# Kernel optimization log

Measured on AMD Instinct MI355X. Metric: run time of the kernel, lower is better.

The kernel has to match this reference:

```python
import jax, jax.numpy as jnp
import numpy as np

EMBED_DIM = 1024
NUM_HEADS = 16
HEAD_DIM = EMBED_DIM // NUM_HEADS
WINDOW = 128  # window_size: attend to [i-W, i+W]


def setup_inputs() -> dict:
    key = jax.random.key(0)
    ks = jax.random.split(key, 9)
    B, S, E = 4, 4096, EMBED_DIM
    s = 1.0 / np.sqrt(E)
    return {
        "x": jax.random.normal(ks[0], (B, S, E), jnp.float32),
        "Wq": jax.random.normal(ks[1], (E, E), jnp.float32) * s,
        "bq": jnp.zeros((E,), jnp.float32),
        "Wk": jax.random.normal(ks[2], (E, E), jnp.float32) * s,
        "bk": jnp.zeros((E,), jnp.float32),
        "Wv": jax.random.normal(ks[3], (E, E), jnp.float32) * s,
        "bv": jnp.zeros((E,), jnp.float32),
        "Wo": jax.random.normal(ks[4], (E, E), jnp.float32) * s,
        "bo": jnp.zeros((E,), jnp.float32),
    }


def reference(x, Wq, bq, Wk, bk, Wv, bv, Wo, bo):
    B, S, E = x.shape
    H, D, W = NUM_HEADS, HEAD_DIM, WINDOW
    scale = jnp.sqrt(jnp.asarray(D, x.dtype))

    def heads(t):  # [B,S,E] -> [B,H,S,D]
        return t.reshape(B, S, H, D).transpose(0, 2, 1, 3)

    q = heads(x @ Wq + bq)
    k = heads(x @ Wk + bk)
    v = heads(x @ Wv + bv)

    # window indices per query position: j = i + [-W..W], masked to [0, S)
    offs = jnp.arange(-W, W + 1)                 # [2W+1]
    idx = jnp.arange(S)[:, None] + offs[None, :]  # [S, 2W+1]
    valid = (idx >= 0) & (idx < S)
    idxc = jnp.clip(idx, 0, S - 1)

    k_win = k[:, :, idxc, :]  # [B,H,S,2W+1,D]
    v_win = v[:, :, idxc, :]

    scores = jnp.einsum('bhsd,bhswd->bhsw', q, k_win) / scale
    scores = jnp.where(valid[None, None], scores, jnp.asarray(-jnp.inf, scores.dtype))
    attn = jax.nn.softmax(scores, axis=-1)
    out = jnp.einsum('bhsw,bhswd->bhsd', attn, v_win)  # [B,H,S,D]

    out = out.transpose(0, 2, 1, 3).reshape(B, S, E)
    return out @ Wo + bo
```

## Files before the change

kernel.cpp:

```cpp
#include <hip/hip_runtime.h>
#include <hip/hip_bf16.h>
#include <type_traits>

typedef unsigned short u16;
typedef __attribute__((ext_vector_type(8))) short  s16x8;
typedef __attribute__((ext_vector_type(4))) short  s16x4;
typedef __attribute__((ext_vector_type(8))) __bf16 b16x8;
typedef __attribute__((ext_vector_type(4))) float  f32x4;

#define S_LEN 4096
#define NB    4
#define EMB   1024
#define NH    16
#define HD    64
#define NROWS (NB * S_LEN)
#define KDIM  1024
#define BHSTRIDE (S_LEN * HD)

static __device__ __forceinline__ u16 f2b(float f) {
  __hip_bfloat16 h = __float2bfloat16(f);
  return __builtin_bit_cast(u16, h);
}

template <typename T, typename = void>
struct mfma_takes : std::false_type {};
template <typename T>
struct mfma_takes<T, std::void_t<decltype(__builtin_amdgcn_mfma_f32_16x16x32_bf16(
    std::declval<T>(), std::declval<T>(), std::declval<f32x4>(), 0, 0, 0))>> : std::true_type {};

template <typename AB>
static __device__ __forceinline__ f32x4 mfma_any(AB a, AB b, f32x4 c) {
  return __builtin_amdgcn_mfma_f32_16x16x32_bf16(a, b, c, 0, 0, 0);
}

template <typename S8 = s16x8, typename B8 = b16x8>
static __device__ __forceinline__ f32x4 MFMA_BF16(s16x8 a, s16x8 b, f32x4 c) {
  if constexpr (mfma_takes<S8>::value)
    return mfma_any<S8>(__builtin_bit_cast(S8, a), __builtin_bit_cast(S8, b), c);
  else
    return mfma_any<B8>(__builtin_bit_cast(B8, a), __builtin_bit_cast(B8, b), c);
}

static __device__ __forceinline__ void gld_lds16(const void* g, void* l) {
  __builtin_amdgcn_global_load_lds((const __attribute__((address_space(1))) void*)g,
                                   (__attribute__((address_space(3))) void*)l, 16, 0, 0);
}

__global__ __launch_bounds__(256) void cvt_x_kernel(const float* __restrict__ in,
                                                    u16* __restrict__ out) {
  long i = ((long)blockIdx.x * 256 + threadIdx.x) * 8;
  float4 a = *(const float4*)(in + i);
  float4 b = *(const float4*)(in + i + 4);
  s16x8 o;
  o[0] = (short)f2b(a.x); o[1] = (short)f2b(a.y); o[2] = (short)f2b(a.z); o[3] = (short)f2b(a.w);
  o[4] = (short)f2b(b.x); o[5] = (short)f2b(b.y); o[6] = (short)f2b(b.z); o[7] = (short)f2b(b.w);
  *(s16x8*)(out + i) = o;
}

__global__ __launch_bounds__(256) void transpose_cvt4_kernel(
    const float* __restrict__ W0, const float* __restrict__ W1,
    const float* __restrict__ W2, const float* __restrict__ W3,
    u16* __restrict__ D0, u16* __restrict__ D1, u16* __restrict__ D2, u16* __restrict__ D3) {
  __shared__ float tile[32][33];
  const float* W; u16* D;
  switch (blockIdx.z) {
    case 0:  W = W0; D = D0; break;
    case 1:  W = W1; D = D1; break;
    case 2:  W = W2; D = D2; break;
    default: W = W3; D = D3; break;
  }
  int n0 = blockIdx.x * 32, k0 = blockIdx.y * 32;
  int tx = threadIdx.x & 31, ty = threadIdx.x >> 5;
#pragma unroll
  for (int i = ty; i < 32; i += 8)
    tile[i][tx] = W[(long)(k0 + i) * EMB + n0 + tx];
  __syncthreads();
#pragma unroll
  for (int i = ty; i < 32; i += 8)
    D[(long)(n0 + i) * EMB + k0 + tx] = f2b(tile[tx][i]);
}

#define SA_(p,k) (((p)*2+(k))*8192)
#define SB_(p,k) (32768 + ((p)*2+(k))*8192)

__global__ __launch_bounds__(512, 2) void gemm8p_kernel(
    const u16* __restrict__ A, const u16* __restrict__ Bt,
    const float* __restrict__ b0, const float* __restrict__ b1, const float* __restrict__ b2,
    void* __restrict__ Cp, u16* __restrict__ Qb, u16* __restrict__ Kp, u16* __restrict__ Vt,
    int N, int out_f32) {
  __shared__ __align__(16) u16 smem[65536];
  const int tid = threadIdx.x;
  const int w = tid >> 6, lane = tid & 63;
  const int wm = w >> 2, wn = w & 3;
  const int frow = lane & 15, fg = lane >> 4;

  const int nwg = gridDim.x;
  const int bid = ((int)blockIdx.x & 7) * (nwg >> 3) + ((int)blockIdx.x >> 3);
  const int nbn = N >> 8;
  const int bm = bid / nbn, bn = bid % nbn;

  int offA[8];
#pragma unroll
  for (int j = 0; j < 8; j++) {
    int row = wm * 128 + j * 16 + frow;
    offA[j] = row * 32 + ((fg ^ ((row ^ (row >> 2)) & 3)) << 3);
  }
  int offB[4];
#pragma unroll
  for (int j = 0; j < 4; j++) {
    int row = wn * 64 + j * 16 + frow;
    offB[j] = row * 32 + ((fg ^ ((row ^ (row >> 2)) & 3)) << 3);
  }
  int srow[2], soff[2];
#pragma unroll
  for (int L = 0; L < 2; L++) {
    int lin = L * 512 + tid;
    int r = lin >> 2;
    srow[L] = r;
    soff[L] = (((lin & 3) ^ ((r ^ (r >> 2)) & 3)) << 3);
  }
  const u16* Abase = A + (long)bm * 256 * KDIM;
  const u16* Bbase = Bt + (long)bn * 256 * KDIM;

  f32x4 acc[8][4];
#pragma unroll
  for (int m = 0; m < 8; m++)
#pragma unroll
    for (int n = 0; n < 4; n++) acc[m][n] = (f32x4)0.0f;

  auto STAGE = [&](const u16* gb, int kcol, int slot) {
#pragma unroll
    for (int L = 0; L < 2; L++)
      gld_lds16(gb + (long)srow[L] * KDIM + kcol + soff[L],
                &smem[slot + (L * 512 + w * 64) * 8]);
  };

  s16x8 af[4], bf[4];

  STAGE(Abase, 0,  SA_(0,0)); STAGE(Bbase, 0,  SB_(0,0));
  STAGE(Abase, 32, SA_(0,1)); STAGE(Bbase, 32, SB_(0,1));
  STAGE(Abase, 64, SA_(1,0)); STAGE(Bbase, 64, SB_(1,0));
  asm volatile("s_waitcnt vmcnt(8)" ::: "memory");
  asm volatile("s_barrier" ::: "memory");

#define PHASE(p, k, mh, RDB, GB, KCOL, SLOT, DOVM)                            \
  {                                                                           \
    if (RDB) {                                                                \
      _Pragma("unroll") for (int n = 0; n < 4; n++)                           \
        bf[n] = *(const s16x8*)&smem[SB_(p, k) + offB[n]];                    \
    }                                                                         \
    _Pragma("unroll") for (int m = 0; m < 4; m++)                             \
      af[m] = *(const s16x8*)&smem[SA_(p, k) + offA[(mh) * 4 + m]];           \
    STAGE(GB, KCOL, SLOT);                                                    \
    asm volatile("s_barrier" ::: "memory");                                   \
    asm volatile("s_waitcnt lgkmcnt(0)" ::: "memory");                        \
    __builtin_amdgcn_sched_barrier(0);                                        \
    __builtin_amdgcn_s_setprio(1);                                            \
    _Pragma("unroll") for (int m = 0; m < 4; m++)                             \
      _Pragma("unroll") for (int n = 0; n < 4; n++)                           \
        acc[(mh) * 4 + m][n] = MFMA_BF16(af[m], bf[n], acc[(mh) * 4 + m][n]); \
    __builtin_amdgcn_s_setprio(0);                                            \
    if (DOVM) asm volatile("s_waitcnt vmcnt(8)" ::: "memory");                \
    asm volatile("s_barrier" ::: "memory");                                   \
  }

#pragma unroll 1
  for (int i = 0; i < 8; i++) {
    const int t = 2 * i;
    const int k1 = ((t + 1) & 15) * 64;
    const int k2 = ((t + 2) & 15) * 64;
    const int k3 = ((t + 3) & 15) * 64;
    PHASE(0, 0, 0, 1, Abase, k1 + 32, SA_(1, 1), 0)
    PHASE(0, 0, 1, 0, Bbase, k1 + 32, SB_(1, 1), 1)
    PHASE(0, 1, 0, 1, Abase, k2,      SA_(0, 0), 0)
    PHASE(0, 1, 1, 0, Bbase, k2,      SB_(0, 0), 1)
    PHASE(1, 0, 0, 1, Abase, k2 + 32, SA_(0, 1), 0)
    PHASE(1, 0, 1, 0, Bbase, k2 + 32, SB_(0, 1), 1)
    PHASE(1, 1, 0, 1, Abase, k3,      SA_(1, 0), 0)
    PHASE(1, 1, 1, 0, Bbase, k3,      SB_(1, 0), 1)
  }
#undef PHASE

  asm volatile("s_waitcnt vmcnt(0) lgkmcnt(0)" ::: "memory");
  asm volatile("s_barrier" ::: "memory");

  const int Mbase = bm * 256 + wm * 128;

  if (!out_f32) {
    const int g = bn * 256 + wn * 64;
    const int part = g >> 10;
    const int head = (g & 1023) >> 6;
    const float* bias = (part == 0) ? b0 : ((part == 1) ? b1 : b2);
    float bv[4];
#pragma unroll
    for (int n = 0; n < 4; n++) bv[n] = bias[(g & 1023) + n * 16 + frow];
    u16* buf = &smem[w * 2048];
#pragma unroll
    for (int mf2 = 0; mf2 < 4; mf2++) {
#pragma unroll
      for (int half = 0; half < 2; half++) {
        const int mf = mf2 * 2 + half;
#pragma unroll
        for (int n = 0; n < 4; n++)
#pragma unroll
          for (int r = 0; r < 4; r++) {
            int row32 = half * 16 + 4 * fg + r;
            int col = n * 16 + frow;
            buf[row32 * 64 + (((col >> 3) ^ (row32 & 7)) << 3) + (col & 7)] =
                f2b(acc[mf][n][r] + bv[n]);
          }
      }
      asm volatile("s_waitcnt lgkmcnt(0)" ::: "memory");
      __builtin_amdgcn_sched_barrier(0);
      const int s0 = Mbase + mf2 * 32;
      if (part == 2) {
        const int d = lane;
        u16 tmp[32];
#pragma unroll
        for (int r32 = 0; r32 < 32; r32++)
          tmp[r32] = buf[r32 * 64 + (((d >> 3) ^ (r32 & 7)) << 3) + (d & 7)];
        u16* dst = Vt + ((long)((s0 >> 12) * 16 + head)) * BHSTRIDE + (long)d * S_LEN + (s0 & 4095);
#pragma unroll
        for (int q = 0; q < 4; q++) {
          s16x8 pk;
#pragma unroll
          for (int j = 0; j < 8; j++) pk[j] = (short)tmp[q * 8 + j];
          *(s16x8*)(dst + q * 8) = pk;
        }
      } else {
#pragma unroll
        for (int i = 0; i < 4; i++) {
          int flat = lane + 64 * i;
          int row32 = flat >> 3, ch = flat & 7;
          s16x8 v = *(const s16x8*)&buf[row32 * 64 + ((ch ^ (row32 & 7)) << 3)];
          int s = s0 + row32;
          u16* dst = (part == 0)
              ? (Qb + (long)s * 1024 + head * 64 + ch * 8)
              : (Kp + ((long)(s >> 12) * 16 + head) * BHSTRIDE + (long)(s & 4095) * 64 + ch * 8);
          *(s16x8*)dst = v;
        }
      }
      asm volatile("s_waitcnt lgkmcnt(0)" ::: "memory");
      __builtin_amdgcn_sched_barrier(0);
    }
  } else {
    float* fbuf = (float*)&smem[w * 2048];
    const long crow0 = (long)Mbase * N + bn * 256 + wn * 64;
#pragma unroll
    for (int mf = 0; mf < 8; mf++) {
#pragma unroll
      for (int n = 0; n < 4; n++) {
        float bvv = b0[(bn * 256 + wn * 64 + n * 16 + frow) & 1023];
#pragma unroll
        for (int r = 0; r < 4; r++) {
          int row = 4 * fg + r;
          int o = 4 * n + (frow >> 2);
          fbuf[row * 64 + ((o ^ (row & 7)) << 2) + (frow & 3)] = acc[mf][n][r] + bvv;
        }
      }
      asm volatile("s_waitcnt lgkmcnt(0)" ::: "memory");
      __builtin_amdgcn_sched_barrier(0);
#pragma unroll
      for (int i = 0; i < 4; i++) {
        int flat = lane + 64 * i;
        int row = flat >> 4, oct = lane & 15;
        float4 v = *(const float4*)&fbuf[row * 64 + ((oct ^ (row & 7)) << 2)];
        *(float4*)((float*)Cp + crow0 + (long)(mf * 16 + row) * N + oct * 4) = v;
      }
      asm volatile("s_waitcnt lgkmcnt(0)" ::: "memory");
      __builtin_amdgcn_sched_barrier(0);
    }
  }
}

#define QBLK 128

__global__ __launch_bounds__(256) void attn_kernel(const u16* __restrict__ Qb,
                                                   const u16* __restrict__ Kp,
                                                   const u16* __restrict__ Vt,
                                                   u16* __restrict__ Oa) {
  __shared__ __align__(16) u16 smem[16384];

  const int tid = threadIdx.x;
  const int w = tid >> 6, lane = tid & 63;
  const int frow = lane & 15, fg = lane >> 4;

  const int nq = S_LEN / QBLK;
  int bid = (int)blockIdx.x;
  bid = (bid & 7) * ((NB * NH * nq) >> 3) + (bid >> 3);
  const int b = bid / (NH * nq);
  const int rem = bid % (NH * nq);
  const int h = rem / nq;
  const int qt = rem % nq;
  const int q0 = qt * QBLK;
  const int qw0 = q0 + 32 * w;

  const u16* Kpb = Kp + (long)(b * NH + h) * BHSTRIDE;
  const u16* Vtb = Vt + (long)(b * NH + h) * BHSTRIDE;

  s16x8 qf[2][2];
#pragma unroll
  for (int m = 0; m < 2; m++)
#pragma unroll
    for (int kk = 0; kk < 2; kk++)
      qf[m][kk] = *(const s16x8*)(Qb + (long)(b * S_LEN + qw0 + 16 * m + frow) * 1024 +
                                  h * 64 + kk * 32 + 8 * fg);

  f32x4 acc[2][4];
#pragma unroll
  for (int m = 0; m < 2; m++)
#pragma unroll
    for (int n = 0; n < 4; n++) acc[m][n] = (f32x4)0.0f;
  float mrow[2] = {-1e30f, -1e30f};
  float lrow[2] = {0.f, 0.f};

  const int r8 = lane >> 3;
  const int cs = ((lane & 7) ^ r8) << 3;

  auto STAGE = [&](int kvb, int bufi) {
#pragma unroll
    for (int pass = 0; pass < 2; pass++) {
      int rbase = pass * 32 + w * 8;
      gld_lds16(Kpb + (long)(kvb + rbase + r8) * 64 + cs, &smem[bufi * 4096 + rbase * 64]);
      gld_lds16(Vtb + (long)(rbase + r8) * S_LEN + kvb + cs, &smem[8192 + bufi * 4096 + rbase * 64]);
    }
  };

  const int tlo = (q0 == 0) ? 2 : 0;
  const int thi = (q0 == S_LEN - QBLK) ? 3 : 5;

  STAGE(q0 - 128 + 64 * tlo, 0);

#pragma unroll 1
  for (int t = tlo; t <= thi; t++) {
    const int cur = (t - tlo) & 1;
    const int kvb = q0 - 128 + 64 * t;
    if (t < thi) {
      STAGE(kvb + 64, cur ^ 1);
      asm volatile("s_waitcnt vmcnt(4)" ::: "memory");
    } else {
      asm volatile("s_waitcnt vmcnt(0)" ::: "memory");
    }
    asm volatile("s_barrier" ::: "memory");

    const bool active = (kvb + 63 >= qw0 - 128) && (kvb <= qw0 + 159);
    if (active) {
      const u16* lK = &smem[cur * 4096];
      const u16* lV = &smem[8192 + cur * 4096];
      f32x4 sfr[2][4];
#pragma unroll
      for (int m = 0; m < 2; m++)
#pragma unroll
        for (int n = 0; n < 4; n++) sfr[m][n] = (f32x4)0.0f;
#pragma unroll
      for (int kk = 0; kk < 2; kk++) {
        s16x8 kb[4];
#pragma unroll
        for (int n = 0; n < 4; n++)
          kb[n] = *(const s16x8*)&lK[(16 * n + frow) * 64 + (((fg + 4 * kk) ^ (frow & 7)) << 3)];
#pragma unroll
        for (int m = 0; m < 2; m++)
#pragma unroll
          for (int n = 0; n < 4; n++)
            sfr[m][n] = MFMA_BF16(kb[n], qf[m][kk], sfr[m][n]);
      }
#pragma unroll
      for (int m = 0; m < 2; m++) {
        const int dbase = kvb - (qw0 + 16 * m + frow) + 128 + 4 * fg;
        float tmax = -1e30f;
#pragma unroll
        for (int n = 0; n < 4; n++)
#pragma unroll
          for (int r = 0; r < 4; r++) {
            bool valid = (unsigned)(dbase + 16 * n + r) <= 256u;
            float xv = valid ? sfr[m][n][r] * 0.125f : -1e30f;
            sfr[m][n][r] = xv;
            tmax = fmaxf(tmax, xv);
          }
        tmax = fmaxf(tmax, __shfl_xor(tmax, 16));
        tmax = fmaxf(tmax, __shfl_xor(tmax, 32));
        float mold = mrow[m];
        float mnew = fmaxf(mold, tmax);
        float al = __expf(mold - mnew);
        mrow[m] = mnew;
        float ps = 0.f;
#pragma unroll
        for (int n = 0; n < 4; n++)
#pragma unroll
          for (int r = 0; r < 4; r++) {
            float e = (sfr[m][n][r] > -1e29f) ? __expf(sfr[m][n][r] - mnew) : 0.f;
            sfr[m][n][r] = e;
            ps += e;
          }
        ps += __shfl_xor(ps, 16);
        ps += __shfl_xor(ps, 32);
        lrow[m] = lrow[m] * al + ps;
        float a4[4];
#pragma unroll
        for (int r = 0; r < 4; r++) a4[r] = __shfl(al, 20 * fg + r);
#pragma unroll
        for (int nd = 0; nd < 4; nd++)
#pragma unroll
          for (int r = 0; r < 4; r++) acc[m][nd][r] *= a4[r];
      }
      s16x8 pa[2][2];
#pragma unroll
      for (int m = 0; m < 2; m++)
#pragma unroll
        for (int kt = 0; kt < 2; kt++)
#pragma unroll
          for (int j = 0; j < 8; j++)
            pa[m][kt][j] = (short)f2b(sfr[m][2 * kt + (j >> 2)][j & 3]);
#pragma unroll
      for (int kt = 0; kt < 2; kt++)
#pragma unroll
        for (int nd = 0; nd < 4; nd++) {
          const int d = 16 * nd + frow;
          const int key = frow & 7;
          const int olo = (4 * kt + (fg >> 1)) ^ key;
          const int ohi = (4 * kt + 2 + (fg >> 1)) ^ key;
          s16x4 lo = *(const s16x4*)&lV[d * 64 + olo * 8 + (fg & 1) * 4];
          s16x4 hi = *(const s16x4*)&lV[d * 64 + ohi * 8 + (fg & 1) * 4];
          s16x8 vb;
          vb[0] = lo[0]; vb[1] = lo[1]; vb[2] = lo[2]; vb[3] = lo[3];
          vb[4] = hi[0]; vb[5] = hi[1]; vb[6] = hi[2]; vb[7] = hi[3];
#pragma unroll
          for (int m = 0; m < 2; m++)
            acc[m][nd] = MFMA_BF16(pa[m][kt], vb, acc[m][nd]);
        }
    }
    asm volatile("s_barrier" ::: "memory");
  }

  float i4[2][4];
#pragma unroll
  for (int m = 0; m < 2; m++) {
    float inv = 1.0f / lrow[m];
#pragma unroll
    for (int r = 0; r < 4; r++) i4[m][r] = __shfl(inv, 20 * fg + r);
  }
  u16* bb = &smem[w * 2048];
#pragma unroll
  for (int m = 0; m < 2; m++)
#pragma unroll
    for (int nd = 0; nd < 4; nd++)
#pragma unroll
      for (int r = 0; r < 4; r++) {
        int row32 = 16 * m + 4 * fg + r;
        int col = 16 * nd + frow;
        bb[row32 * 64 + (((col >> 3) ^ (row32 & 7)) << 3) + (col & 7)] =
            f2b(acc[m][nd][r] * i4[m][r]);
      }
  asm volatile("s_waitcnt lgkmcnt(0)" ::: "memory");
  __builtin_amdgcn_sched_barrier(0);
  u16* Ob = Oa + ((long)(b * S_LEN + qw0)) * EMB + h * HD;
#pragma unroll
  for (int i = 0; i < 4; i++) {
    int flat = lane + 64 * i;
    int row32 = flat >> 3, ch = flat & 7;
    s16x8 v = *(const s16x8*)&bb[row32 * 64 + ((ch ^ (row32 & 7)) << 3)];
    *(s16x8*)(Ob + (long)row32 * EMB + ch * 8) = v;
  }
}

extern "C" void kernel_launch(void* const* d_in, const int* in_sizes, int n_in,
                              void* d_out, int out_size, void* d_ws, size_t ws_size,
                              hipStream_t stream) {
  const float* x  = (const float*)d_in[0];
  const float* Wq = (const float*)d_in[1];
  const float* bq = (const float*)d_in[2];
  const float* Wk = (const float*)d_in[3];
  const float* bk = (const float*)d_in[4];
  const float* Wv = (const float*)d_in[5];
  const float* bv = (const float*)d_in[6];
  const float* Wo = (const float*)d_in[7];
  const float* bo = (const float*)d_in[8];

  char* ws = (char*)d_ws;
  u16* xb   = (u16*)ws;  ws += (size_t)NROWS * EMB * 2;
  u16* Wt   = (u16*)ws;  ws += (size_t)3 * EMB * EMB * 2;
  u16* Wot  = (u16*)ws;  ws += (size_t)EMB * EMB * 2;
  u16* Qbuf = (u16*)ws;  ws += (size_t)NROWS * EMB * 2;
  u16* Kpb  = (u16*)ws;  ws += (size_t)NB * NH * BHSTRIDE * 2;
  u16* Vtb  = (u16*)ws;  ws += (size_t)NB * NH * BHSTRIDE * 2;
  u16* Oab  = (u16*)ws;  ws += (size_t)NROWS * EMB * 2;

  cvt_x_kernel<<<(NROWS * EMB) / (256 * 8), 256, 0, stream>>>(x, xb);

  dim3 tg(EMB / 32, EMB / 32, 4);
  transpose_cvt4_kernel<<<tg, 256, 0, stream>>>(
      Wq, Wk, Wv, Wo, Wt, Wt + (size_t)EMB * EMB, Wt + (size_t)2 * EMB * EMB, Wot);

  gemm8p_kernel<<<(NROWS / 256) * (3 * EMB / 256), 512, 0, stream>>>(
      xb, Wt, bq, bk, bv, nullptr, Qbuf, Kpb, Vtb, 3 * EMB, 0);

  attn_kernel<<<NB * NH * (S_LEN / QBLK), 256, 0, stream>>>(Qbuf, Kpb, Vtb, Oab);

  gemm8p_kernel<<<(NROWS / 256) * (EMB / 256), 512, 0, stream>>>(
      Oab, Wot, bo, bo, bo, d_out, nullptr, nullptr, nullptr, EMB, 1);
}
```

Baseline: 252.1 us.

## Write V transposed directly from registers and skip softmax rescale when max stable

In the QKV projection epilogue, the V part now writes transposed bf16 values straight from MFMA accumulators to global memory in 4-element chunks, bypassing the LDS staging and per-lane gather. In the attention kernel, the online softmax only rescales the running max, sum and output accumulator when some row's new max exceeds the old by more than a threshold (a lazy rescale). This removes most exp and multiply work per tile, and the masked-score check is dropped because masked entries underflow to zero in exp. The risks are narrower global stores for V and a looser numerical bound on exponent growth.

```diff
diff --git a/kernel.cpp b/kernel.cpp
--- a/kernel.cpp
+++ b/kernel.cpp
@@ -194,40 +194,43 @@
     float bv[4];
 #pragma unroll
     for (int n = 0; n < 4; n++) bv[n] = bias[(g & 1023) + n * 16 + frow];
-    u16* buf = &smem[w * 2048];
-#pragma unroll
-    for (int mf2 = 0; mf2 < 4; mf2++) {
-#pragma unroll
-      for (int half = 0; half < 2; half++) {
-        const int mf = mf2 * 2 + half;
-#pragma unroll
-        for (int n = 0; n < 4; n++)
-#pragma unroll
-          for (int r = 0; r < 4; r++) {
-            int row32 = half * 16 + 4 * fg + r;
-            int col = n * 16 + frow;
-            buf[row32 * 64 + (((col >> 3) ^ (row32 & 7)) << 3) + (col & 7)] =
-                f2b(acc[mf][n][r] + bv[n]);
-          }
-      }
-      asm volatile("s_waitcnt lgkmcnt(0)" ::: "memory");
-      __builtin_amdgcn_sched_barrier(0);
-      const int s0 = Mbase + mf2 * 32;
-      if (part == 2) {
-        const int d = lane;
-        u16 tmp[32];
-#pragma unroll
-        for (int r32 = 0; r32 < 32; r32++)
-          tmp[r32] = buf[r32 * 64 + (((d >> 3) ^ (r32 & 7)) << 3) + (d & 7)];
-        u16* dst = Vt + ((long)((s0 >> 12) * 16 + head)) * BHSTRIDE + (long)d * S_LEN + (s0 & 4095);
-#pragma unroll
-        for (int q = 0; q < 4; q++) {
-          s16x8 pk;
-#pragma unroll
-          for (int j = 0; j < 8; j++) pk[j] = (short)tmp[q * 8 + j];
-          *(s16x8*)(dst + q * 8) = pk;
+
+    if (part == 2) {
+      const int batch = Mbase >> 12;
+      const int sl0 = (Mbase & 4095) + 4 * fg;
+      u16* dstb = Vt + ((long)(batch * 16 + head)) * BHSTRIDE + sl0;
+#pragma unroll
+      for (int n = 0; n < 4; n++) {
+        const int d = n * 16 + frow;
+        u16* dr = dstb + (long)d * S_LEN;
+#pragma unroll
+        for (int mf = 0; mf < 8; mf++) {
+          s16x4 pk;
+#pragma unroll
+          for (int r = 0; r < 4; r++) pk[r] = (short)f2b(acc[mf][n][r] + bv[n]);
+          *(s16x4*)(dr + mf * 16) = pk;
         }
-      } else {
+      }
+    } else {
+      u16* buf = &smem[w * 2048];
+#pragma unroll
+      for (int mf2 = 0; mf2 < 4; mf2++) {
+#pragma unroll
+        for (int half = 0; half < 2; half++) {
+          const int mf = mf2 * 2 + half;
+#pragma unroll
+          for (int n = 0; n < 4; n++)
+#pragma unroll
+            for (int r = 0; r < 4; r++) {
+              int row32 = half * 16 + 4 * fg + r;
+              int col = n * 16 + frow;
+              buf[row32 * 64 + (((col >> 3) ^ (row32 & 7)) << 3) + (col & 7)] =
+                  f2b(acc[mf][n][r] + bv[n]);
+            }
+        }
+        asm volatile("s_waitcnt lgkmcnt(0)" ::: "memory");
+        __builtin_amdgcn_sched_barrier(0);
+        const int s0 = Mbase + mf2 * 32;
 #pragma unroll
         for (int i = 0; i < 4; i++) {
           int flat = lane + 64 * i;
@@ -239,9 +242,9 @@
               : (Kp + ((long)(s >> 12) * 16 + head) * BHSTRIDE + (long)(s & 4095) * 64 + ch * 8);
           *(s16x8*)dst = v;
         }
-      }
-      asm volatile("s_waitcnt lgkmcnt(0)" ::: "memory");
-      __builtin_amdgcn_sched_barrier(0);
+        asm volatile("s_waitcnt lgkmcnt(0)" ::: "memory");
+        __builtin_amdgcn_sched_barrier(0);
+      }
     }
   } else {
     float* fbuf = (float*)&smem[w * 2048];
@@ -379,29 +382,31 @@
           }
         tmax = fmaxf(tmax, __shfl_xor(tmax, 16));
         tmax = fmaxf(tmax, __shfl_xor(tmax, 32));
-        float mold = mrow[m];
-        float mnew = fmaxf(mold, tmax);
-        float al = __expf(mold - mnew);
-        mrow[m] = mnew;
+        if (!__all(tmax - mrow[m] <= 8.0f)) {
+          float mnew = fmaxf(mrow[m], tmax);
+          float al = __expf(mrow[m] - mnew);
+          mrow[m] = mnew;
+          lrow[m] *= al;
+          float a4[4];
+#pragma unroll
+          for (int r = 0; r < 4; r++) a4[r] = __shfl(al, 20 * fg + r);
+#pragma unroll
+          for (int nd = 0; nd < 4; nd++)
+#pragma unroll
+            for (int r = 0; r < 4; r++) acc[m][nd][r] *= a4[r];
+        }
         float ps = 0.f;
 #pragma unroll
         for (int n = 0; n < 4; n++)
 #pragma unroll
           for (int r = 0; r < 4; r++) {
-            float e = (sfr[m][n][r] > -1e29f) ? __expf(sfr[m][n][r] - mnew) : 0.f;
+            float e = __expf(sfr[m][n][r] - mrow[m]);
             sfr[m][n][r] = e;
             ps += e;
           }
         ps += __shfl_xor(ps, 16);
         ps += __shfl_xor(ps, 32);
-        lrow[m] = lrow[m] * al + ps;
-        float a4[4];
-#pragma unroll
-        for (int r = 0; r < 4; r++) a4[r] = __shfl(al, 20 * fg + r);
-#pragma unroll
-        for (int nd = 0; nd < 4; nd++)
-#pragma unroll
-          for (int r = 0; r < 4; r++) acc[m][nd][r] *= a4[r];
+        lrow[m] += ps;
       }
       s16x8 pa[2][2];
 #pragma unroll
```

Result: no change. 248.0 us (-1.6%).
